# Performance work log

Hardware: AMD Instinct MI355X
Metric: run time of the kernel (lower is better)

The kernel has to match this reference:

```python
import jax, jax.numpy as jnp
import numpy as np

# ---- hyperparameters (from init_kwargs) ----
SIGMA, RHO = 1.0, 10.0
ALPHA, BETA = 1.0, 1.0
K = 3  # ksize; patches are non-overlapping KxK, structure tensor computed on each patch
GRAY_W = np.array([0.2989, 0.587, 0.114], dtype=np.float32)  # torchvision Grayscale weights


def _gauss1d(sigma):
    d = np.arange(-1.0, 2.0, dtype=np.float32)  # radius-1 kernel (fits 3x3 patches)
    g = np.exp(-d * d / (2.0 * sigma * sigma))
    return (g / g.sum()).astype(np.float32)


def _dgauss1d(sigma):
    d = np.arange(-1.0, 2.0, dtype=np.float32)
    g = _gauss1d(sigma)
    return (-d / (sigma * sigma) * g).astype(np.float32)


def _conv3(x, k2d):
    # 'same' zero-padded 3x3 correlation over the last two dims, fully broadcast
    H, W = x.shape[-2], x.shape[-1]
    xp = jnp.pad(x, [(0, 0)] * (x.ndim - 2) + [(1, 1), (1, 1)])
    out = jnp.zeros_like(x)
    for i in range(3):
        for j in range(3):
            out = out + k2d[i, j] * xp[..., i:i + H, j:j + W]
    return out


# precomputed separable kernels (numpy constants)
_G_S, _DG_S, _G_R = _gauss1d(SIGMA), _dgauss1d(SIGMA), _gauss1d(RHO)
_KX = np.outer(_G_S, _DG_S)   # d/dx (last axis), gaussian-smoothed
_KY = np.outer(_DG_S, _G_S)   # d/dy
_KS = np.outer(_G_R, _G_R)    # rho smoothing


def _structure_tensor(gray):
    # gray: (..., K, K) -> (..., 3, K, K) components (Jxx, Jyy, Jxy)
    Ix = _conv3(gray, _KX)
    Iy = _conv3(gray, _KY)
    Jxx = _conv3(Ix * Ix, _KS)
    Jyy = _conv3(Iy * Iy, _KS)
    Jxy = _conv3(Ix * Iy, _KS)
    return jnp.stack([Jxx, Jyy, Jxy], axis=-3)


def _compute_patches(img):
    # img: (B, 3, H, W) -> (B, P, 3*K*K); non-overlapping KxK patches,
    # grayscale -> structure tensor -> per-patch L2 normalize (vectorized, no vmap-of-tiny-ops)
    B, C, H, W = img.shape
    Hb, Wb = H // K, W // K
    p = img.reshape(B, C, Hb, K, Wb, K).transpose(0, 2, 4, 1, 3, 5)  # (B,Hb,Wb,3,K,K)
    p = p.reshape(B, Hb * Wb, C, K, K)
    gray = jnp.einsum('bpchw,c->bphw', p, jnp.asarray(GRAY_W, p.dtype))
    st = _structure_tensor(gray)                                      # (B,P,3,K,K)
    n = jnp.sqrt(jnp.sum(st * st, axis=(-3, -2, -1), keepdims=True)) + 1e-12
    st = st / n
    return st.reshape(B, Hb * Wb, 3 * K * K)


def _resize(img, factor):
    B, C, H, W = img.shape
    return jax.image.resize(img, (B, C, int(H * factor), int(W * factor)),
                            method='bicubic', antialias=False)


def _pairdist_sq(a, b):
    # squared L2 pairwise distance (monotone in L2; only used for argmin)
    aa = jnp.sum(a * a, axis=-1)[:, :, None]
    bb = jnp.sum(b * b, axis=-1)[:, None, :]
    ab = jnp.einsum('bnw,bmw->bnm', a, b)
    return aa + bb - 2.0 * ab


def _loss(x, gt):
    p1 = _compute_patches(x)
    p2 = _compute_patches(gt)
    p2_2 = _compute_patches(_resize(gt, 0.5))
    p2_4 = _compute_patches(_resize(gt, 0.25))
    p2c = jnp.concatenate([p2, p2_2, p2_4], axis=1)      # (B, P2cat, 27)
    score = ALPHA * _pairdist_sq(p1, p2c) + BETA * _pairdist_sq(p2, p2c)
    ind = jnp.argmin(score, axis=2)                      # (B, P1) nearest-neighbor indices
    sel = jnp.take_along_axis(p2c, ind[:, :, None], axis=1)
    return jnp.mean(jnp.abs(p1 - sel))                   # L1 criterion


def setup_inputs() -> dict:
    key = jax.random.key(0)
    k1, k2 = jax.random.split(key)
    x = jax.random.uniform(k1, (4, 3, 192, 192), dtype=jnp.float32)
    gt = jax.random.uniform(k2, (4, 3, 192, 192), dtype=jnp.float32)
    return {'x': x, 'gt': gt}


def reference(x, gt):
    return _loss(x, gt)
```

## Files before the change

### kernel.cpp

```cpp
#include <hip/hip_runtime.h>
#include <hip/hip_bf16.h>
#include <math.h>

namespace {
constexpr int BATCH = 4;
constexpr int IMG   = 192;
constexpr int PL    = IMG * IMG;
constexpr int NP1   = 4096;
constexpr int MALL  = 5376;
constexpr int RS    = 28;
constexpr int NCHUNK = 16;
constexpr int TPC    = 21;

#define GA 0.27406862f
#define GB 0.45186276f
#define RC 0.33277732f
#define RD 0.33444537f

typedef __bf16 bf16x8 __attribute__((ext_vector_type(8)));
typedef float  f32x4  __attribute__((ext_vector_type(4)));

__device__ __forceinline__ void conv3(const float in[9], const float k[9], float out[9]) {
#pragma unroll
  for (int y = 0; y < 3; ++y)
#pragma unroll
    for (int x = 0; x < 3; ++x) {
      float s = 0.f;
#pragma unroll
      for (int i = 0; i < 3; ++i) {
        int yy = y + i - 1;
        if (yy < 0 || yy > 2) continue;
#pragma unroll
        for (int j = 0; j < 3; ++j) {
          int xx = x + j - 1;
          if (xx < 0 || xx > 2) continue;
          s = fmaf(k[i * 3 + j], in[yy * 3 + xx], s);
        }
      }
      out[y * 3 + x] = s;
    }
}

__device__ __forceinline__ void st_from_gray(const float gray[9], float stv[27], float& cs) {
  const float KX[9] = {GA * GA, 0.f, -GA * GA, GB * GA, 0.f, -GB * GA, GA * GA, 0.f, -GA * GA};
  const float KY[9] = {GA * GA, GA * GB, GA * GA, 0.f, 0.f, 0.f, -GA * GA, -GA * GB, -GA * GA};
  const float KS[9] = {RC * RC, RC * RD, RC * RC, RD * RC, RD * RD, RD * RC, RC * RC, RC * RD, RC * RC};
  float Ix[9], Iy[9];
  conv3(gray, KX, Ix);
  conv3(gray, KY, Iy);
  float Pxx[9], Pyy[9], Pxy[9];
#pragma unroll
  for (int t = 0; t < 9; ++t) {
    Pxx[t] = Ix[t] * Ix[t];
    Pyy[t] = Iy[t] * Iy[t];
    Pxy[t] = Ix[t] * Iy[t];
  }
  conv3(Pxx, KS, stv + 0);
  conv3(Pyy, KS, stv + 9);
  conv3(Pxy, KS, stv + 18);
  float s2 = 0.f;
#pragma unroll
  for (int d = 0; d < 27; ++d) s2 = fmaf(stv[d], stv[d], s2);
  float inv = 1.0f / (sqrtf(s2) + 1e-12f);
  float c = 0.f;
#pragma unroll
  for (int d = 0; d < 27; ++d) {
    stv[d] *= inv;
    c = fmaf(stv[d], stv[d], c);
  }
  cs = c;
}

__device__ __forceinline__ void mkw(int k0, int IS, float w[4], int k[4]) {
  const float W4[4] = {-0.0625f, 0.5625f, 0.5625f, -0.0625f};
  float ssum = 0.f;
#pragma unroll
  for (int u = 0; u < 4; ++u) {
    int kk = k0 + u;
    bool v = (kk >= 0) && (kk < IS);
    w[u] = v ? W4[u] : 0.f;
    k[u] = v ? kk : 0;
    ssum += w[u];
  }
  float inv = 1.f / ssum;
#pragma unroll
  for (int u = 0; u < 4; ++u) w[u] *= inv;
}

__device__ __forceinline__ float bicubic_gray(const float* __restrict__ im,
                                              int i, int j, int step, int koff) {
  float wr[4], wc[4];
  int kr[4], kc[4];
  mkw(step * i + koff, IMG, wr, kr);
  mkw(step * j + koff, IMG, wc, kc);
  float acc = 0.f;
#pragma unroll
  for (int u = 0; u < 4; ++u) {
    float rs = 0.f;
#pragma unroll
    for (int v = 0; v < 4; ++v) {
      int o = kr[u] * IMG + kc[v];
      float gy = fmaf(0.114f, im[2 * PL + o], fmaf(0.587f, im[PL + o], 0.2989f * im[o]));
      rs = fmaf(wc[v], gy, rs);
    }
    acc = fmaf(wr[u], rs, acc);
  }
  return acc;
}

__device__ __forceinline__ void pack_row_frag(const float* __restrict__ v, float tail,
                                              unsigned* __restrict__ base, int rl) {
  unsigned uh[16], ul[16];
#pragma unroll
  for (int p = 0; p < 16; ++p) {
    float a  = (2 * p < 27) ? v[2 * p] : 0.f;
    float bb = (2 * p + 1 < 27) ? v[2 * p + 1] : (2 * p + 1 == 27 ? tail : 0.f);
    __hip_bfloat16 ah = __float2bfloat16(a);
    __hip_bfloat16 bh = __float2bfloat16(bb);
    float af = __bfloat162float(ah), bf2 = __bfloat162float(bh);
    __hip_bfloat16 al = __float2bfloat16(a - af);
    __hip_bfloat16 bl = __float2bfloat16(bb - bf2);
    uh[p] = ((unsigned)__builtin_bit_cast(unsigned short, bh) << 16) |
            (unsigned)__builtin_bit_cast(unsigned short, ah);
    ul[p] = ((unsigned)__builtin_bit_cast(unsigned short, bl) << 16) |
            (unsigned)__builtin_bit_cast(unsigned short, al);
  }
#pragma unroll
  for (int lg = 0; lg < 4; ++lg) {
    *reinterpret_cast<uint4*>(base + (size_t)(lg * 16 + rl) * 4) =
        make_uint4(uh[4 * lg], uh[4 * lg + 1], uh[4 * lg + 2], uh[4 * lg + 3]);
    *reinterpret_cast<uint4*>(base + 256 + (size_t)(lg * 16 + rl) * 4) =
        make_uint4(ul[4 * lg], ul[4 * lg + 1], ul[4 * lg + 2], ul[4 * lg + 3]);
  }
}

__device__ __forceinline__ void store_row28(float* __restrict__ dst, const float v[27], float tail) {
  float4* d4 = reinterpret_cast<float4*>(dst);
#pragma unroll
  for (int i = 0; i < 6; ++i)
    d4[i] = make_float4(v[4 * i], v[4 * i + 1], v[4 * i + 2], v[4 * i + 3]);
  d4[6] = make_float4(v[24], v[25], v[26], tail);
}

__global__ void __launch_bounds__(256) prep_all_kernel(
    const float* __restrict__ x, const float* __restrict__ gt,
    float* __restrict__ p1, float* __restrict__ p2c,
    unsigned* __restrict__ Cp, unsigned* __restrict__ ctr) {
  const int bid = blockIdx.x;
  const int t = threadIdx.x;
  if (bid == 0 && t == 0) ctr[0] = 0;

  if (bid < 128) {
    const bool isx = bid < 64;
    const int gid = (isx ? bid : bid - 64) * 256 + t;
    const int b = gid >> 12, p = gid & (NP1 - 1);
    const int hb = p >> 6, wb = p & 63;
    const float* base = (isx ? x : gt) + (size_t)b * 3 * PL + (size_t)(hb * 3) * IMG + wb * 3;
    float gr[9];
#pragma unroll
    for (int y = 0; y < 3; ++y)
#pragma unroll
      for (int xx = 0; xx < 3; ++xx) {
        int o = y * IMG + xx;
        gr[y * 3 + xx] = fmaf(0.114f, base[2 * PL + o],
                              fmaf(0.587f, base[PL + o], 0.2989f * base[o]));
      }
    float s[27];
    float cs;
    st_from_gray(gr, s, cs);
    if (isx) {
      store_row28(p1 + (size_t)gid * RS, s, cs);
    } else {
      size_t crow = (size_t)b * MALL + p;
      store_row28(p2c + crow * RS, s, cs);
      pack_row_frag(s, -cs, Cp + (crow >> 4) * 512, (int)(crow & 15));
    }
  } else {
    int row;
    float gr[9];
    if (bid < 144) {
      int q = (bid - 128) * 256 + t;
      int b = q >> 10, p = q & 1023;
      int hb = p >> 5, wb = p & 31;
      const float* im = gt + (size_t)b * 3 * PL;
#pragma unroll
      for (int y = 0; y < 3; ++y)
#pragma unroll
        for (int xx = 0; xx < 3; ++xx)
          gr[y * 3 + xx] = bicubic_gray(im, 3 * hb + y, 3 * wb + xx, 2, -1);
      row = b * MALL + NP1 + p;
    } else {
      int q = (bid - 144) * 256 + t;
      int b = q >> 8, p = q & 255;
      int hb = p >> 4, wb = p & 15;
      const float* im = gt + (size_t)b * 3 * PL;
#pragma unroll
      for (int y = 0; y < 3; ++y)
#pragma unroll
        for (int xx = 0; xx < 3; ++xx)
          gr[y * 3 + xx] = bicubic_gray(im, 3 * hb + y, 3 * wb + xx, 4, 0);
      row = b * MALL + NP1 + 1024 + p;
    }
    float s[27];
    float cs;
    st_from_gray(gr, s, cs);
    store_row28(p2c + (size_t)row * RS, s, cs);
    pack_row_frag(s, -cs, Cp + ((size_t)row >> 4) * 512, row & 15);
  }
}

__global__ void __launch_bounds__(256) pack_q_kernel(
    const float* __restrict__ p1, const float* __restrict__ p2c,
    unsigned* __restrict__ Qp) {
  int gid = blockIdx.x * 256 + threadIdx.x;
  int b = gid >> 12, n = gid & (NP1 - 1);
  const float* a = p1 + (size_t)gid * RS;
  const float* c = p2c + ((size_t)b * MALL + n) * RS;
  float v[27];
#pragma unroll
  for (int d = 0; d < 27; ++d) v[d] = a[d] + c[d];
  pack_row_frag(v, 1.0f, Qp + (size_t)(gid >> 4) * 512, gid & 15);
}

__global__ void __launch_bounds__(256) argmin_mfma_kernel(
    const unsigned* __restrict__ Qp, const unsigned* __restrict__ Cp,
    unsigned* __restrict__ pkey, int* __restrict__ pidx) {
  const int lane = threadIdx.x & 63;
  const int w = threadIdx.x >> 6;
  const int chunk = blockIdx.y;
  const int b = blockIdx.z;
  const int nbase = blockIdx.x * 256 + w * 64;
  const int lm = lane & 15, lg = lane >> 4;

  __shared__ unsigned cbuf[2][512];

  bf16x8 qh[4], ql[4];
#pragma unroll
  for (int t = 0; t < 4; ++t) {
    const unsigned* tb = Qp + (size_t)((b * NP1 + nbase) >> 4) * 512 + (size_t)t * 512 + lane * 4;
    qh[t] = *reinterpret_cast<const bf16x8*>(tb);
    ql[t] = *reinterpret_cast<const bf16x8*>(tb + 256);
  }

  unsigned keys[4][4];
#pragma unroll
  for (int t = 0; t < 4; ++t)
#pragma unroll
    for (int r = 0; r < 4; ++r) keys[t][r] = 0u;

  const int tile0 = chunk * TPC;
  const unsigned* ct = Cp + (size_t)(b * (MALL >> 4) + tile0) * 512;

  {
    uint2 s0 = *reinterpret_cast<const uint2*>(ct + 2 * threadIdx.x);
    *reinterpret_cast<uint2*>(&cbuf[0][2 * threadIdx.x]) = s0;
  }
  __syncthreads();

  for (int i = 0; i < TPC; ++i) {
    uint2 nx;
    if (i + 1 < TPC)
      nx = *reinterpret_cast<const uint2*>(ct + (size_t)(i + 1) * 512 + 2 * threadIdx.x);

    const unsigned* cb = &cbuf[i & 1][0];
    bf16x8 ch = *reinterpret_cast<const bf16x8*>(cb + lane * 4);
    bf16x8 cl = *reinterpret_cast<const bf16x8*>(cb + 256 + lane * 4);
    const unsigned tag = (unsigned)(TPC - 1 - i);
#pragma unroll
    for (int t = 0; t < 4; ++t) {
      f32x4 a = {4.f, 4.f, 4.f, 4.f};
      a = __builtin_amdgcn_mfma_f32_16x16x32_bf16(qh[t], ch, a, 0, 0, 0);
      a = __builtin_amdgcn_mfma_f32_16x16x32_bf16(ql[t], ch, a, 0, 0, 0);
      a = __builtin_amdgcn_mfma_f32_16x16x32_bf16(qh[t], cl, a, 0, 0, 0);
#pragma unroll
      for (int r = 0; r < 4; ++r) {
        unsigned kb = (__builtin_bit_cast(unsigned, (float)a[r]) & 0xFFFFFFE0u) | tag;
        keys[t][r] = keys[t][r] > kb ? keys[t][r] : kb;
      }
    }
    if (i + 1 < TPC) {
      __syncthreads();
      *reinterpret_cast<uint2*>(&cbuf[(i + 1) & 1][2 * threadIdx.x]) = nx;
      __syncthreads();
    }
  }

#pragma unroll
  for (int t = 0; t < 4; ++t)
#pragma unroll
    for (int r = 0; r < 4; ++r) {
      unsigned k = keys[t][r];
      int m = (tile0 + (int)((unsigned)(TPC - 1) - (k & 31u))) * 16 + lm;
#pragma unroll
      for (int mk = 1; mk < 16; mk <<= 1) {
        unsigned ok = (unsigned)__shfl_xor((int)k, mk, 64);
        int om = __shfl_xor(m, mk, 64);
        bool take = (ok > k) || (ok == k && om < m);
        k = take ? ok : k;
        m = take ? om : m;
      }
      if (lm == 0) {
        int row = nbase + t * 16 + lg * 4 + r;
        size_t o = ((size_t)(b * NP1 + row)) * NCHUNK + chunk;
        pkey[o] = k & 0xFFFFFFE0u;
        pidx[o] = m;
      }
    }
}

__global__ void __launch_bounds__(256) finalize_kernel(
    const float* __restrict__ p1, const float* __restrict__ p2c,
    const unsigned* __restrict__ pkey, const int* __restrict__ pidx,
    float* __restrict__ bsum, unsigned* __restrict__ ctr, float* __restrict__ out) {
  int g = blockIdx.x * 256 + threadIdx.x;
  unsigned bk = 0u;
  int bi = 0;
  for (int ms = 0; ms < NCHUNK; ++ms) {
    unsigned k = pkey[(size_t)g * NCHUNK + ms];
    int ix = pidx[(size_t)g * NCHUNK + ms];
    bool gg = k > bk;
    bk = gg ? k : bk;
    bi = gg ? ix : bi;
  }
  int b = g >> 12;
  const float* a = p1 + (size_t)g * RS;
  const float* s2 = p2c + ((size_t)b * MALL + bi) * RS;
  float acc = 0.f;
#pragma unroll
  for (int d = 0; d < 27; ++d) acc += fabsf(a[d] - s2[d]);

  __shared__ float red[256];
  red[threadIdx.x] = acc;
  __syncthreads();
  for (int st = 128; st > 0; st >>= 1) {
    if (threadIdx.x < st) red[threadIdx.x] += red[threadIdx.x + st];
    __syncthreads();
  }
  if (threadIdx.x == 0) {
    __hip_atomic_store(&bsum[blockIdx.x], red[0], __ATOMIC_RELEASE, __HIP_MEMORY_SCOPE_AGENT);
    unsigned prev = __hip_atomic_fetch_add(ctr, 1u, __ATOMIC_ACQ_REL, __HIP_MEMORY_SCOPE_AGENT);
    if (prev == 63) {
      float s = 0.f;
      for (int i = 0; i < 64; ++i)
        s += __hip_atomic_load(&bsum[i], __ATOMIC_ACQUIRE, __HIP_MEMORY_SCOPE_AGENT);
      out[0] = s * (1.0f / 442368.0f);
    }
  }
}

}

extern "C" void kernel_launch(void* const* d_in, const int* in_sizes, int n_in,
                              void* d_out, int out_size, void* d_ws, size_t ws_size,
                              hipStream_t stream) {
  const float* x  = (const float*)d_in[0];
  const float* gt = (const float*)d_in[1];
  float* out = (float*)d_out;

  float* ws = (float*)d_ws;
  float* p1   = ws;
  float* p2c  = p1 + (size_t)BATCH * NP1 * RS;
  unsigned* Qp = (unsigned*)(p2c + (size_t)BATCH * MALL * RS);
  unsigned* Cp = Qp + (size_t)BATCH * NP1 * 32;
  unsigned* pkey = Cp + (size_t)BATCH * MALL * 32 + 512;
  int*   pidx   = (int*)(pkey + (size_t)BATCH * NP1 * NCHUNK);
  float* bsum   = (float*)(pidx + (size_t)BATCH * NP1 * NCHUNK);
  unsigned* ctr = (unsigned*)(bsum + 64);

  prep_all_kernel<<<148, 256, 0, stream>>>(x, gt, p1, p2c, Cp, ctr);

  pack_q_kernel<<<64, 256, 0, stream>>>(p1, p2c, Qp);

  {
    dim3 grid(16, NCHUNK, BATCH);
    argmin_mfma_kernel<<<grid, 256, 0, stream>>>(Qp, Cp, pkey, pidx);
  }

  finalize_kernel<<<64, 256, 0, stream>>>(p1, p2c, pkey, pidx, bsum, ctr, out);
}
```

Measured before the change: 60.65 us.

## Precompute grayscale and resized images, fuse Q packing, batch C tiles per round

Splits preprocessing into a grayscale pass and a separate bicubic-resize pass that works on gray images, so the resize no longer recomputes grayscale for every tap. The patch kernel now builds p1, p2c, Cp and Qp in one launch, which removes the separate pack_q kernel. The argmin kernel regroups chunks as 21 chunks of 16 tiles, loads 4 tiles per round to cut barriers, and stores partial keys chunk-major so the finalize kernel reads them coalesced. The cost is an extra kernel launch and global round trips for the gray images.

```diff
diff --git a/kernel.cpp b/kernel.cpp
--- a/kernel.cpp
+++ b/kernel.cpp
@@ -9,8 +9,11 @@
 constexpr int NP1   = 4096;
 constexpr int MALL  = 5376;
 constexpr int RS    = 28;
-constexpr int NCHUNK = 16;
-constexpr int TPC    = 21;
+constexpr int NCHUNK = 21;
+constexpr int TPC    = 16;
+constexpr int RPT    = 4;
+constexpr int ROUNDS = TPC / RPT;
+constexpr int NROWS  = BATCH * NP1;
 
 #define GA 0.27406862f
 #define GB 0.45186276f
@@ -85,27 +88,6 @@
   float inv = 1.f / ssum;
 #pragma unroll
   for (int u = 0; u < 4; ++u) w[u] *= inv;
-}
-
-__device__ __forceinline__ float bicubic_gray(const float* __restrict__ im,
-                                              int i, int j, int step, int koff) {
-  float wr[4], wc[4];
-  int kr[4], kc[4];
-  mkw(step * i + koff, IMG, wr, kr);
-  mkw(step * j + koff, IMG, wc, kc);
-  float acc = 0.f;
-#pragma unroll
-  for (int u = 0; u < 4; ++u) {
-    float rs = 0.f;
-#pragma unroll
-    for (int v = 0; v < 4; ++v) {
-      int o = kr[u] * IMG + kc[v];
-      float gy = fmaf(0.114f, im[2 * PL + o], fmaf(0.587f, im[PL + o], 0.2989f * im[o]));
-      rs = fmaf(wc[v], gy, rs);
-    }
-    acc = fmaf(wr[u], rs, acc);
-  }
-  return acc;
 }
 
 __device__ __forceinline__ void pack_row_frag(const float* __restrict__ v, float tail,
@@ -142,65 +124,118 @@
   d4[6] = make_float4(v[24], v[25], v[26], tail);
 }
 
-__global__ void __launch_bounds__(256) prep_all_kernel(
+__global__ void __launch_bounds__(256) gray_kernel(
     const float* __restrict__ x, const float* __restrict__ gt,
+    float* __restrict__ gx, float* __restrict__ ggt, unsigned* __restrict__ ctr) {
+  int o = blockIdx.x * 256 + threadIdx.x;
+  if (o == 0) ctr[0] = 0;
+  const float* src;
+  float* dst;
+  int oo;
+  if (o < BATCH * PL) { src = x; dst = gx; oo = o; }
+  else                { src = gt; dst = ggt; oo = o - BATCH * PL; }
+  int b = oo / PL, p = oo - b * PL;
+  const float* im = src + (size_t)b * 3 * PL;
+  dst[oo] = fmaf(0.114f, im[2 * PL + p], fmaf(0.587f, im[PL + p], 0.2989f * im[p]));
+}
+
+__global__ void __launch_bounds__(256) resize_gray_kernel(
+    const float* __restrict__ ggt, float* __restrict__ g96, float* __restrict__ g48) {
+  int o = blockIdx.x * 256 + threadIdx.x;
+  int i, j, S, step, koff;
+  const float* src;
+  float* dst;
+  int oo;
+  if (o < BATCH * 9216) {
+    int b = o / 9216, rem = o - b * 9216;
+    i = rem / 96; j = rem - i * 96;
+    S = 96; step = 2; koff = -1;
+    src = ggt + (size_t)b * PL;
+    dst = g96; oo = o;
+  } else {
+    int q = o - BATCH * 9216;
+    int b = q / 2304, rem = q - b * 2304;
+    i = rem / 48; j = rem - i * 48;
+    S = 48; step = 4; koff = 0;
+    src = ggt + (size_t)b * PL;
+    dst = g48; oo = q;
+  }
+  (void)S;
+  float wr[4], wc[4];
+  int kr[4], kc[4];
+  mkw(step * i + koff, IMG, wr, kr);
+  mkw(step * j + koff, IMG, wc, kc);
+  float acc = 0.f;
+#pragma unroll
+  for (int u = 0; u < 4; ++u) {
+    float rs = 0.f;
+#pragma unroll
+    for (int v = 0; v < 4; ++v) rs = fmaf(wc[v], src[kr[u] * IMG + kc[v]], rs);
+    acc = fmaf(wr[u], rs, acc);
+  }
+  dst[oo] = acc;
+}
+
+__global__ void __launch_bounds__(256) patch_all_kernel(
+    const float* __restrict__ gx, const float* __restrict__ ggt,
+    const float* __restrict__ g96, const float* __restrict__ g48,
     float* __restrict__ p1, float* __restrict__ p2c,
-    unsigned* __restrict__ Cp, unsigned* __restrict__ ctr) {
-  const int bid = blockIdx.x;
-  const int t = threadIdx.x;
-  if (bid == 0 && t == 0) ctr[0] = 0;
-
-  if (bid < 128) {
-    const bool isx = bid < 64;
-    const int gid = (isx ? bid : bid - 64) * 256 + t;
-    const int b = gid >> 12, p = gid & (NP1 - 1);
-    const int hb = p >> 6, wb = p & 63;
-    const float* base = (isx ? x : gt) + (size_t)b * 3 * PL + (size_t)(hb * 3) * IMG + wb * 3;
+    unsigned* __restrict__ Qp, unsigned* __restrict__ Cp) {
+  int g = blockIdx.x * 256 + threadIdx.x;
+  if (g < NROWS) {
+    int b = g >> 12, p = g & (NP1 - 1);
+    int hb = p >> 6, wb = p & 63;
+    const int off = (hb * 3) * IMG + wb * 3;
     float gr[9];
+    const float* gp = gx + (size_t)b * PL + off;
 #pragma unroll
     for (int y = 0; y < 3; ++y)
 #pragma unroll
-      for (int xx = 0; xx < 3; ++xx) {
-        int o = y * IMG + xx;
-        gr[y * 3 + xx] = fmaf(0.114f, base[2 * PL + o],
-                              fmaf(0.587f, base[PL + o], 0.2989f * base[o]));
-      }
-    float s[27];
-    float cs;
-    st_from_gray(gr, s, cs);
-    if (isx) {
-      store_row28(p1 + (size_t)gid * RS, s, cs);
-    } else {
-      size_t crow = (size_t)b * MALL + p;
-      store_row28(p2c + crow * RS, s, cs);
-      pack_row_frag(s, -cs, Cp + (crow >> 4) * 512, (int)(crow & 15));
-    }
+      for (int xx = 0; xx < 3; ++xx) gr[y * 3 + xx] = gp[y * IMG + xx];
+    float s1[27];
+    float cs1;
+    st_from_gray(gr, s1, cs1);
+    store_row28(p1 + (size_t)g * RS, s1, cs1);
+
+    const float* hp = ggt + (size_t)b * PL + off;
+#pragma unroll
+    for (int y = 0; y < 3; ++y)
+#pragma unroll
+      for (int xx = 0; xx < 3; ++xx) gr[y * 3 + xx] = hp[y * IMG + xx];
+    float s2[27];
+    float cs2;
+    st_from_gray(gr, s2, cs2);
+    size_t crow = (size_t)b * MALL + p;
+    store_row28(p2c + crow * RS, s2, cs2);
+    pack_row_frag(s2, -cs2, Cp + (crow >> 4) * 512, (int)(crow & 15));
+
+    float q[27];
+#pragma unroll
+    for (int d = 0; d < 27; ++d) q[d] = s1[d] + s2[d];
+    pack_row_frag(q, 1.0f, Qp + (size_t)(g >> 4) * 512, g & 15);
   } else {
-    int row;
-    float gr[9];
-    if (bid < 144) {
-      int q = (bid - 128) * 256 + t;
+    int q = g - NROWS;
+    const float* src;
+    int S, row, hb, wb;
+    if (q < BATCH * 1024) {
       int b = q >> 10, p = q & 1023;
-      int hb = p >> 5, wb = p & 31;
-      const float* im = gt + (size_t)b * 3 * PL;
-#pragma unroll
-      for (int y = 0; y < 3; ++y)
-#pragma unroll
-        for (int xx = 0; xx < 3; ++xx)
-          gr[y * 3 + xx] = bicubic_gray(im, 3 * hb + y, 3 * wb + xx, 2, -1);
+      hb = p >> 5; wb = p & 31;
+      src = g96 + (size_t)b * 9216;
+      S = 96;
       row = b * MALL + NP1 + p;
     } else {
-      int q = (bid - 144) * 256 + t;
-      int b = q >> 8, p = q & 255;
-      int hb = p >> 4, wb = p & 15;
-      const float* im = gt + (size_t)b * 3 * PL;
-#pragma unroll
-      for (int y = 0; y < 3; ++y)
-#pragma unroll
-        for (int xx = 0; xx < 3; ++xx)
-          gr[y * 3 + xx] = bicubic_gray(im, 3 * hb + y, 3 * wb + xx, 4, 0);
+      int q2 = q - BATCH * 1024;
+      int b = q2 >> 8, p = q2 & 255;
+      hb = p >> 4; wb = p & 15;
+      src = g48 + (size_t)b * 2304;
+      S = 48;
       row = b * MALL + NP1 + 1024 + p;
     }
+    float gr[9];
+#pragma unroll
+    for (int y = 0; y < 3; ++y)
+#pragma unroll
+      for (int xx = 0; xx < 3; ++xx) gr[y * 3 + xx] = src[(3 * hb + y) * S + 3 * wb + xx];
     float s[27];
     float cs;
     st_from_gray(gr, s, cs);
@@ -209,30 +244,18 @@
   }
 }
 
-__global__ void __launch_bounds__(256) pack_q_kernel(
-    const float* __restrict__ p1, const float* __restrict__ p2c,
-    unsigned* __restrict__ Qp) {
-  int gid = blockIdx.x * 256 + threadIdx.x;
-  int b = gid >> 12, n = gid & (NP1 - 1);
-  const float* a = p1 + (size_t)gid * RS;
-  const float* c = p2c + ((size_t)b * MALL + n) * RS;
-  float v[27];
-#pragma unroll
-  for (int d = 0; d < 27; ++d) v[d] = a[d] + c[d];
-  pack_row_frag(v, 1.0f, Qp + (size_t)(gid >> 4) * 512, gid & 15);
-}
-
 __global__ void __launch_bounds__(256) argmin_mfma_kernel(
     const unsigned* __restrict__ Qp, const unsigned* __restrict__ Cp,
     unsigned* __restrict__ pkey, int* __restrict__ pidx) {
   const int lane = threadIdx.x & 63;
   const int w = threadIdx.x >> 6;
+  const int td = threadIdx.x;
   const int chunk = blockIdx.y;
   const int b = blockIdx.z;
   const int nbase = blockIdx.x * 256 + w * 64;
   const int lm = lane & 15, lg = lane >> 4;
 
-  __shared__ unsigned cbuf[2][512];
+  __shared__ unsigned cbuf[2][RPT * 512];
 
   bf16x8 qh[4], ql[4];
 #pragma unroll
@@ -252,35 +275,43 @@
   const unsigned* ct = Cp + (size_t)(b * (MALL >> 4) + tile0) * 512;
 
   {
-    uint2 s0 = *reinterpret_cast<const uint2*>(ct + 2 * threadIdx.x);
-    *reinterpret_cast<uint2*>(&cbuf[0][2 * threadIdx.x]) = s0;
+    uint4 a0 = *reinterpret_cast<const uint4*>(ct + 8 * td);
+    uint4 a1 = *reinterpret_cast<const uint4*>(ct + 8 * td + 4);
+    *reinterpret_cast<uint4*>(&cbuf[0][8 * td]) = a0;
+    *reinterpret_cast<uint4*>(&cbuf[0][8 * td + 4]) = a1;
   }
   __syncthreads();
 
-  for (int i = 0; i < TPC; ++i) {
-    uint2 nx;
-    if (i + 1 < TPC)
-      nx = *reinterpret_cast<const uint2*>(ct + (size_t)(i + 1) * 512 + 2 * threadIdx.x);
-
-    const unsigned* cb = &cbuf[i & 1][0];
-    bf16x8 ch = *reinterpret_cast<const bf16x8*>(cb + lane * 4);
-    bf16x8 cl = *reinterpret_cast<const bf16x8*>(cb + 256 + lane * 4);
-    const unsigned tag = (unsigned)(TPC - 1 - i);
-#pragma unroll
-    for (int t = 0; t < 4; ++t) {
-      f32x4 a = {4.f, 4.f, 4.f, 4.f};
-      a = __builtin_amdgcn_mfma_f32_16x16x32_bf16(qh[t], ch, a, 0, 0, 0);
-      a = __builtin_amdgcn_mfma_f32_16x16x32_bf16(ql[t], ch, a, 0, 0, 0);
-      a = __builtin_amdgcn_mfma_f32_16x16x32_bf16(qh[t], cl, a, 0, 0, 0);
-#pragma unroll
-      for (int r = 0; r < 4; ++r) {
-        unsigned kb = (__builtin_bit_cast(unsigned, (float)a[r]) & 0xFFFFFFE0u) | tag;
-        keys[t][r] = keys[t][r] > kb ? keys[t][r] : kb;
+  for (int r = 0; r < ROUNDS; ++r) {
+    uint4 n0, n1;
+    if (r + 1 < ROUNDS) {
+      n0 = *reinterpret_cast<const uint4*>(ct + (size_t)(r + 1) * (RPT * 512) + 8 * td);
+      n1 = *reinterpret_cast<const uint4*>(ct + (size_t)(r + 1) * (RPT * 512) + 8 * td + 4);
+    }
+    const unsigned* cbr = &cbuf[r & 1][0];
+#pragma unroll
+    for (int it = 0; it < RPT; ++it) {
+      const int i = r * RPT + it;
+      bf16x8 ch = *reinterpret_cast<const bf16x8*>(cbr + it * 512 + lane * 4);
+      bf16x8 cl = *reinterpret_cast<const bf16x8*>(cbr + it * 512 + 256 + lane * 4);
+      const unsigned tag = (unsigned)(TPC - 1 - i);
+#pragma unroll
+      for (int t = 0; t < 4; ++t) {
+        f32x4 a = {4.f, 4.f, 4.f, 4.f};
+        a = __builtin_amdgcn_mfma_f32_16x16x32_bf16(qh[t], ch, a, 0, 0, 0);
+        a = __builtin_amdgcn_mfma_f32_16x16x32_bf16(ql[t], ch, a, 0, 0, 0);
+        a = __builtin_amdgcn_mfma_f32_16x16x32_bf16(qh[t], cl, a, 0, 0, 0);
+#pragma unroll
+        for (int rr = 0; rr < 4; ++rr) {
+          unsigned kb = (__builtin_bit_cast(unsigned, (float)a[rr]) & 0xFFFFFFE0u) | tag;
+          keys[t][rr] = keys[t][rr] > kb ? keys[t][rr] : kb;
+        }
       }
     }
-    if (i + 1 < TPC) {
+    if (r + 1 < ROUNDS) {
       __syncthreads();
-      *reinterpret_cast<uint2*>(&cbuf[(i + 1) & 1][2 * threadIdx.x]) = nx;
+      *reinterpret_cast<uint4*>(&cbuf[(r + 1) & 1][8 * td]) = n0;
+      *reinterpret_cast<uint4*>(&cbuf[(r + 1) & 1][8 * td + 4]) = n1;
       __syncthreads();
     }
   }
@@ -301,7 +332,7 @@
       }
       if (lm == 0) {
         int row = nbase + t * 16 + lg * 4 + r;
-        size_t o = ((size_t)(b * NP1 + row)) * NCHUNK + chunk;
+        size_t o = (size_t)chunk * NROWS + b * NP1 + row;
         pkey[o] = k & 0xFFFFFFE0u;
         pidx[o] = m;
       }
@@ -316,8 +347,8 @@
   unsigned bk = 0u;
   int bi = 0;
   for (int ms = 0; ms < NCHUNK; ++ms) {
-    unsigned k = pkey[(size_t)g * NCHUNK + ms];
-    int ix = pidx[(size_t)g * NCHUNK + ms];
+    unsigned k = pkey[(size_t)ms * NROWS + g];
+    int ix = pidx[(size_t)ms * NROWS + g];
     bool gg = k > bk;
     bk = gg ? k : bk;
     bi = gg ? ix : bi;
@@ -362,14 +393,21 @@
   float* p2c  = p1 + (size_t)BATCH * NP1 * RS;
   unsigned* Qp = (unsigned*)(p2c + (size_t)BATCH * MALL * RS);
   unsigned* Cp = Qp + (size_t)BATCH * NP1 * 32;
-  unsigned* pkey = Cp + (size_t)BATCH * MALL * 32 + 512;
-  int*   pidx   = (int*)(pkey + (size_t)BATCH * NP1 * NCHUNK);
-  float* bsum   = (float*)(pidx + (size_t)BATCH * NP1 * NCHUNK);
+  float* gx   = (float*)(Cp + (size_t)BATCH * MALL * 32);
+  float* ggt  = gx + (size_t)BATCH * PL;
+  float* g96  = ggt + (size_t)BATCH * PL;
+  float* g48  = g96 + (size_t)BATCH * 9216;
+  unsigned* pkey = (unsigned*)(g48 + (size_t)BATCH * 2304);
+  int*   pidx   = (int*)(pkey + (size_t)NCHUNK * NROWS);
+  float* bsum   = (float*)(pidx + (size_t)NCHUNK * NROWS);
   unsigned* ctr = (unsigned*)(bsum + 64);
 
-  prep_all_kernel<<<148, 256, 0, stream>>>(x, gt, p1, p2c, Cp, ctr);
-
-  pack_q_kernel<<<64, 256, 0, stream>>>(p1, p2c, Qp);
+  gray_kernel<<<(2 * BATCH * PL) / 256, 256, 0, stream>>>(x, gt, gx, ggt, ctr);
+
+  resize_gray_kernel<<<(BATCH * (9216 + 2304)) / 256, 256, 0, stream>>>(ggt, g96, g48);
+
+  patch_all_kernel<<<(NROWS + BATCH * 1280) / 256, 256, 0, stream>>>(
+      gx, ggt, g96, g48, p1, p2c, Qp, Cp);
 
   {
     dim3 grid(16, NCHUNK, BATCH);
```

Result: slower. 83.91 us (+38.3%).

## Triple-buffer candidate tiles, widen chunk split, transpose partial-result layout

Applied to the files above, without the earlier changes.

The argmin kernel now splits candidates into 28 chunks of 12 tiles instead of 16 of 21, which gives more blocks for parallelism. It stages two tiles per round through a three-deep LDS ring with a prefetch distance of two, so each round needs one barrier instead of two per tile. MFMA work is wrapped in s_setprio. The partial key/index arrays are stored chunk-major so the finalize kernel reads them coalesced, at the cost of more partials to reduce.

```diff
diff --git a/kernel.cpp b/kernel.cpp
--- a/kernel.cpp
+++ b/kernel.cpp
@@ -9,8 +9,12 @@
 constexpr int NP1   = 4096;
 constexpr int MALL  = 5376;
 constexpr int RS    = 28;
-constexpr int NCHUNK = 16;
-constexpr int TPC    = 21;
+constexpr int NCHUNK = 28;
+constexpr int TPC    = 12;
+constexpr int RPT    = 2;
+constexpr int ROUNDS = TPC / RPT;
+constexpr int NBUF   = 3;
+constexpr int NROWS  = BATCH * NP1;
 
 #define GA 0.27406862f
 #define GB 0.45186276f
@@ -227,12 +231,13 @@
     unsigned* __restrict__ pkey, int* __restrict__ pidx) {
   const int lane = threadIdx.x & 63;
   const int w = threadIdx.x >> 6;
+  const int td = threadIdx.x;
   const int chunk = blockIdx.y;
   const int b = blockIdx.z;
   const int nbase = blockIdx.x * 256 + w * 64;
   const int lm = lane & 15, lg = lane >> 4;
 
-  __shared__ unsigned cbuf[2][512];
+  __shared__ unsigned cbuf[NBUF][RPT * 512];
 
   bf16x8 qh[4], ql[4];
 #pragma unroll
@@ -251,38 +256,51 @@
   const int tile0 = chunk * TPC;
   const unsigned* ct = Cp + (size_t)(b * (MALL >> 4) + tile0) * 512;
 
-  {
-    uint2 s0 = *reinterpret_cast<const uint2*>(ct + 2 * threadIdx.x);
-    *reinterpret_cast<uint2*>(&cbuf[0][2 * threadIdx.x]) = s0;
+#pragma unroll
+  for (int p = 0; p < 2; ++p) {
+    uint2 a0 = *reinterpret_cast<const uint2*>(ct + (size_t)p * 1024 + 2 * td);
+    uint2 a1 = *reinterpret_cast<const uint2*>(ct + (size_t)p * 1024 + 512 + 2 * td);
+    *reinterpret_cast<uint2*>(&cbuf[p][2 * td]) = a0;
+    *reinterpret_cast<uint2*>(&cbuf[p][512 + 2 * td]) = a1;
   }
   __syncthreads();
 
-  for (int i = 0; i < TPC; ++i) {
-    uint2 nx;
-    if (i + 1 < TPC)
-      nx = *reinterpret_cast<const uint2*>(ct + (size_t)(i + 1) * 512 + 2 * threadIdx.x);
-
-    const unsigned* cb = &cbuf[i & 1][0];
-    bf16x8 ch = *reinterpret_cast<const bf16x8*>(cb + lane * 4);
-    bf16x8 cl = *reinterpret_cast<const bf16x8*>(cb + 256 + lane * 4);
-    const unsigned tag = (unsigned)(TPC - 1 - i);
-#pragma unroll
-    for (int t = 0; t < 4; ++t) {
-      f32x4 a = {4.f, 4.f, 4.f, 4.f};
-      a = __builtin_amdgcn_mfma_f32_16x16x32_bf16(qh[t], ch, a, 0, 0, 0);
-      a = __builtin_amdgcn_mfma_f32_16x16x32_bf16(ql[t], ch, a, 0, 0, 0);
-      a = __builtin_amdgcn_mfma_f32_16x16x32_bf16(qh[t], cl, a, 0, 0, 0);
-#pragma unroll
-      for (int r = 0; r < 4; ++r) {
-        unsigned kb = (__builtin_bit_cast(unsigned, (float)a[r]) & 0xFFFFFFE0u) | tag;
-        keys[t][r] = keys[t][r] > kb ? keys[t][r] : kb;
-      }
-    }
-    if (i + 1 < TPC) {
-      __syncthreads();
-      *reinterpret_cast<uint2*>(&cbuf[(i + 1) & 1][2 * threadIdx.x]) = nx;
-      __syncthreads();
-    }
+  for (int r = 0; r < ROUNDS; ++r) {
+    uint2 n0, n1;
+    const bool pf = (r + 2 < ROUNDS);
+    if (pf) {
+      const unsigned* nt = ct + (size_t)(r + 2) * 1024;
+      n0 = *reinterpret_cast<const uint2*>(nt + 2 * td);
+      n1 = *reinterpret_cast<const uint2*>(nt + 512 + 2 * td);
+    }
+    const unsigned* cbr = &cbuf[r % NBUF][0];
+    __builtin_amdgcn_s_setprio(1);
+#pragma unroll
+    for (int it = 0; it < RPT; ++it) {
+      const int i = r * RPT + it;
+      bf16x8 ch = *reinterpret_cast<const bf16x8*>(cbr + it * 512 + lane * 4);
+      bf16x8 cl = *reinterpret_cast<const bf16x8*>(cbr + it * 512 + 256 + lane * 4);
+      const unsigned tag = (unsigned)(TPC - 1 - i);
+#pragma unroll
+      for (int t = 0; t < 4; ++t) {
+        f32x4 a = {4.f, 4.f, 4.f, 4.f};
+        a = __builtin_amdgcn_mfma_f32_16x16x32_bf16(qh[t], ch, a, 0, 0, 0);
+        a = __builtin_amdgcn_mfma_f32_16x16x32_bf16(ql[t], ch, a, 0, 0, 0);
+        a = __builtin_amdgcn_mfma_f32_16x16x32_bf16(qh[t], cl, a, 0, 0, 0);
+#pragma unroll
+        for (int rr = 0; rr < 4; ++rr) {
+          unsigned kb = (__builtin_bit_cast(unsigned, (float)a[rr]) & 0xFFFFFFE0u) | tag;
+          keys[t][rr] = keys[t][rr] > kb ? keys[t][rr] : kb;
+        }
+      }
+    }
+    __builtin_amdgcn_s_setprio(0);
+    if (pf) {
+      unsigned* db = &cbuf[(r + 2) % NBUF][0];
+      *reinterpret_cast<uint2*>(db + 2 * td) = n0;
+      *reinterpret_cast<uint2*>(db + 512 + 2 * td) = n1;
+    }
+    __syncthreads();
   }
 
 #pragma unroll
@@ -301,7 +319,7 @@
       }
       if (lm == 0) {
         int row = nbase + t * 16 + lg * 4 + r;
-        size_t o = ((size_t)(b * NP1 + row)) * NCHUNK + chunk;
+        size_t o = (size_t)chunk * NROWS + b * NP1 + row;
         pkey[o] = k & 0xFFFFFFE0u;
         pidx[o] = m;
       }
@@ -316,8 +334,8 @@
   unsigned bk = 0u;
   int bi = 0;
   for (int ms = 0; ms < NCHUNK; ++ms) {
-    unsigned k = pkey[(size_t)g * NCHUNK + ms];
-    int ix = pidx[(size_t)g * NCHUNK + ms];
+    unsigned k = pkey[(size_t)ms * NROWS + g];
+    int ix = pidx[(size_t)ms * NROWS + g];
     bool gg = k > bk;
     bk = gg ? k : bk;
     bi = gg ? ix : bi;
@@ -362,9 +380,9 @@
   float* p2c  = p1 + (size_t)BATCH * NP1 * RS;
   unsigned* Qp = (unsigned*)(p2c + (size_t)BATCH * MALL * RS);
   unsigned* Cp = Qp + (size_t)BATCH * NP1 * 32;
-  unsigned* pkey = Cp + (size_t)BATCH * MALL * 32 + 512;
-  int*   pidx   = (int*)(pkey + (size_t)BATCH * NP1 * NCHUNK);
-  float* bsum   = (float*)(pidx + (size_t)BATCH * NP1 * NCHUNK);
+  unsigned* pkey = Cp + (size_t)BATCH * MALL * 32;
+  int*   pidx   = (int*)(pkey + (size_t)NCHUNK * NROWS);
+  float* bsum   = (float*)(pidx + (size_t)NCHUNK * NROWS);
   unsigned* ctr = (unsigned*)(bsum + 64);
 
   prep_all_kernel<<<148, 256, 0, stream>>>(x, gt, p1, p2c, Cp, ctr);
```

New measurement: 69.34 us. 14.3% more time.

## Fuse query packing into prep kernel via paired x/gt lanes and shuffles

Applied to the files above, without the earlier changes.

Removes the separate pack_q kernel by interleaving x and gt patches on adjacent lanes in prep_all, so each gt lane gets the matching x structure tensor with shuffles and packs the query row (p1+p2) directly. This drops one kernel launch and the global round trip that re-read p1 and p2c. In exchange, the x and gt loads are now interleaved per lane, which may hurt coalescing, and the gt lanes do extra packing work that leaves the x lanes idle during divergence.

```diff
diff --git a/kernel.cpp b/kernel.cpp
--- a/kernel.cpp
+++ b/kernel.cpp
@@ -11,6 +11,7 @@
 constexpr int RS    = 28;
 constexpr int NCHUNK = 16;
 constexpr int TPC    = 21;
+constexpr int NROWS  = BATCH * NP1;
 
 #define GA 0.27406862f
 #define GB 0.45186276f
@@ -145,62 +146,69 @@
 __global__ void __launch_bounds__(256) prep_all_kernel(
     const float* __restrict__ x, const float* __restrict__ gt,
     float* __restrict__ p1, float* __restrict__ p2c,
-    unsigned* __restrict__ Cp, unsigned* __restrict__ ctr) {
-  const int bid = blockIdx.x;
-  const int t = threadIdx.x;
-  if (bid == 0 && t == 0) ctr[0] = 0;
-
-  if (bid < 128) {
-    const bool isx = bid < 64;
-    const int gid = (isx ? bid : bid - 64) * 256 + t;
-    const int b = gid >> 12, p = gid & (NP1 - 1);
+    unsigned* __restrict__ Qp, unsigned* __restrict__ Cp,
+    unsigned* __restrict__ ctr) {
+  int g = blockIdx.x * 256 + threadIdx.x;
+  if (g == 0) ctr[0] = 0;
+
+  if (g < 2 * NROWS) {
+    const int pid = g >> 1;
+    const bool isgt = g & 1;
+    const int b = pid >> 12, p = pid & (NP1 - 1);
     const int hb = p >> 6, wb = p & 63;
-    const float* base = (isx ? x : gt) + (size_t)b * 3 * PL + (size_t)(hb * 3) * IMG + wb * 3;
+    const float* src = (isgt ? gt : x) + (size_t)b * 3 * PL + (hb * 3) * IMG + wb * 3;
     float gr[9];
 #pragma unroll
     for (int y = 0; y < 3; ++y)
 #pragma unroll
       for (int xx = 0; xx < 3; ++xx) {
         int o = y * IMG + xx;
-        gr[y * 3 + xx] = fmaf(0.114f, base[2 * PL + o],
-                              fmaf(0.587f, base[PL + o], 0.2989f * base[o]));
+        gr[y * 3 + xx] = fmaf(0.114f, src[2 * PL + o],
+                              fmaf(0.587f, src[PL + o], 0.2989f * src[o]));
       }
     float s[27];
     float cs;
     st_from_gray(gr, s, cs);
-    if (isx) {
-      store_row28(p1 + (size_t)gid * RS, s, cs);
+
+    float o27[27];
+#pragma unroll
+    for (int d = 0; d < 27; ++d) o27[d] = __shfl_xor(s[d], 1, 64);
+
+    if (!isgt) {
+      store_row28(p1 + (size_t)pid * RS, s, cs);
     } else {
       size_t crow = (size_t)b * MALL + p;
       store_row28(p2c + crow * RS, s, cs);
       pack_row_frag(s, -cs, Cp + (crow >> 4) * 512, (int)(crow & 15));
+      float q[27];
+#pragma unroll
+      for (int d = 0; d < 27; ++d) q[d] = s[d] + o27[d];
+      pack_row_frag(q, 1.0f, Qp + (size_t)(pid >> 4) * 512, pid & 15);
     }
   } else {
-    int row;
-    float gr[9];
-    if (bid < 144) {
-      int q = (bid - 128) * 256 + t;
+    int q = g - 2 * NROWS;
+    int row, hb, wb, step, koff;
+    const float* im;
+    if (q < BATCH * 1024) {
       int b = q >> 10, p = q & 1023;
-      int hb = p >> 5, wb = p & 31;
-      const float* im = gt + (size_t)b * 3 * PL;
-#pragma unroll
-      for (int y = 0; y < 3; ++y)
-#pragma unroll
-        for (int xx = 0; xx < 3; ++xx)
-          gr[y * 3 + xx] = bicubic_gray(im, 3 * hb + y, 3 * wb + xx, 2, -1);
+      hb = p >> 5; wb = p & 31;
+      im = gt + (size_t)b * 3 * PL;
+      step = 2; koff = -1;
       row = b * MALL + NP1 + p;
     } else {
-      int q = (bid - 144) * 256 + t;
-      int b = q >> 8, p = q & 255;
-      int hb = p >> 4, wb = p & 15;
-      const float* im = gt + (size_t)b * 3 * PL;
-#pragma unroll
-      for (int y = 0; y < 3; ++y)
-#pragma unroll
-        for (int xx = 0; xx < 3; ++xx)
-          gr[y * 3 + xx] = bicubic_gray(im, 3 * hb + y, 3 * wb + xx, 4, 0);
+      int q2 = q - BATCH * 1024;
+      int b = q2 >> 8, p = q2 & 255;
+      hb = p >> 4; wb = p & 15;
+      im = gt + (size_t)b * 3 * PL;
+      step = 4; koff = 0;
       row = b * MALL + NP1 + 1024 + p;
     }
+    float gr[9];
+#pragma unroll
+    for (int y = 0; y < 3; ++y)
+#pragma unroll
+      for (int xx = 0; xx < 3; ++xx)
+        gr[y * 3 + xx] = bicubic_gray(im, 3 * hb + y, 3 * wb + xx, step, koff);
     float s[27];
     float cs;
     st_from_gray(gr, s, cs);
@@ -209,24 +217,12 @@
   }
 }
 
-__global__ void __launch_bounds__(256) pack_q_kernel(
-    const float* __restrict__ p1, const float* __restrict__ p2c,
-    unsigned* __restrict__ Qp) {
-  int gid = blockIdx.x * 256 + threadIdx.x;
-  int b = gid >> 12, n = gid & (NP1 - 1);
-  const float* a = p1 + (size_t)gid * RS;
-  const float* c = p2c + ((size_t)b * MALL + n) * RS;
-  float v[27];
-#pragma unroll
-  for (int d = 0; d < 27; ++d) v[d] = a[d] + c[d];
-  pack_row_frag(v, 1.0f, Qp + (size_t)(gid >> 4) * 512, gid & 15);
-}
-
 __global__ void __launch_bounds__(256) argmin_mfma_kernel(
     const unsigned* __restrict__ Qp, const unsigned* __restrict__ Cp,
     unsigned* __restrict__ pkey, int* __restrict__ pidx) {
   const int lane = threadIdx.x & 63;
   const int w = threadIdx.x >> 6;
+  const int td = threadIdx.x;
   const int chunk = blockIdx.y;
   const int b = blockIdx.z;
   const int nbase = blockIdx.x * 256 + w * 64;
@@ -252,15 +248,15 @@
   const unsigned* ct = Cp + (size_t)(b * (MALL >> 4) + tile0) * 512;
 
   {
-    uint2 s0 = *reinterpret_cast<const uint2*>(ct + 2 * threadIdx.x);
-    *reinterpret_cast<uint2*>(&cbuf[0][2 * threadIdx.x]) = s0;
+    uint2 s0 = *reinterpret_cast<const uint2*>(ct + 2 * td);
+    *reinterpret_cast<uint2*>(&cbuf[0][2 * td]) = s0;
   }
   __syncthreads();
 
   for (int i = 0; i < TPC; ++i) {
     uint2 nx;
     if (i + 1 < TPC)
-      nx = *reinterpret_cast<const uint2*>(ct + (size_t)(i + 1) * 512 + 2 * threadIdx.x);
+      nx = *reinterpret_cast<const uint2*>(ct + (size_t)(i + 1) * 512 + 2 * td);
 
     const unsigned* cb = &cbuf[i & 1][0];
     bf16x8 ch = *reinterpret_cast<const bf16x8*>(cb + lane * 4);
@@ -280,7 +276,7 @@
     }
     if (i + 1 < TPC) {
       __syncthreads();
-      *reinterpret_cast<uint2*>(&cbuf[(i + 1) & 1][2 * threadIdx.x]) = nx;
+      *reinterpret_cast<uint2*>(&cbuf[(i + 1) & 1][2 * td]) = nx;
       __syncthreads();
     }
   }
@@ -363,13 +359,12 @@
   unsigned* Qp = (unsigned*)(p2c + (size_t)BATCH * MALL * RS);
   unsigned* Cp = Qp + (size_t)BATCH * NP1 * 32;
   unsigned* pkey = Cp + (size_t)BATCH * MALL * 32 + 512;
-  int*   pidx   = (int*)(pkey + (size_t)BATCH * NP1 * NCHUNK);
-  float* bsum   = (float*)(pidx + (size_t)BATCH * NP1 * NCHUNK);
+  int*   pidx   = (int*)(pkey + (size_t)NROWS * NCHUNK);
+  float* bsum   = (float*)(pidx + (size_t)NROWS * NCHUNK);
   unsigned* ctr = (unsigned*)(bsum + 64);
 
-  prep_all_kernel<<<148, 256, 0, stream>>>(x, gt, p1, p2c, Cp, ctr);
-
-  pack_q_kernel<<<64, 256, 0, stream>>>(p1, p2c, Qp);
+  prep_all_kernel<<<(2 * NROWS + BATCH * 1280) / 256, 256, 0, stream>>>(
+      x, gt, p1, p2c, Qp, Cp, ctr);
 
   {
     dim3 grid(16, NCHUNK, BATCH);
```

After: 75.17 us. 1.24x slower.
